# Kernel optimization log

Measured on AMD Instinct MI355X. Metric: run time of the kernel, lower is better.

Reference implementation:

```python
import jax, jax.numpy as jnp
import numpy as np

N_ENTITIES = 500_000
N_RELS = 1_000
EMB_DIM = 128
N_TRIPLES = 1_000_000

def setup_inputs() -> dict:
    key = jax.random.key(0)
    k1, k2, k3, k4, k5 = jax.random.split(key, 5)
    memory = jax.random.normal(k1, (N_ENTITIES, EMB_DIM), dtype=jnp.float32) * 0.1
    rel_table = jax.random.normal(k2, (N_RELS, EMB_DIM), dtype=jnp.float32)
    h_idx = jax.random.randint(k3, (N_TRIPLES,), 0, N_ENTITIES, dtype=jnp.int32)
    r_idx = jax.random.randint(k4, (N_TRIPLES,), 0, N_RELS, dtype=jnp.int32)
    t_idx = jax.random.randint(k5, (N_TRIPLES,), 0, N_ENTITIES, dtype=jnp.int32)
    return {"memory": memory, "rel_table": rel_table,
            "h_idx": h_idx, "r_idx": r_idx, "t_idx": t_idx}

def reference(memory, rel_table, h_idx, r_idx, t_idx):
    # Gather (all reads use the OLD memory, matching torch: RHS is computed
    # before the index_put).
    h_vec = memory[h_idx]          # [E, D]
    r_vec = rel_table[r_idx]       # [E, D]
    t_vec = memory[t_idx]          # [E, D]
    msg = h_vec + r_vec - t_vec
    new_vals = 0.9 * h_vec + 0.1 * msg   # = h_vec + 0.1*(r_vec - t_vec)
    # matching torch index_put(accumulate=False) semantics.
    return memory.at[h_idx].set(new_vals)
```

## Files before the change

### kernel.cpp

```cpp
#include <hip/hip_runtime.h>

#define N_ENTITIES 500000
#define N_RELS 1000
#define EMB_DIM 128
#define N_TRIPLES 1000000

typedef float floatx4 __attribute__((ext_vector_type(4)));


__global__ void init_winner_kernel(int* __restrict__ winner) {
    int i = blockIdx.x * blockDim.x + threadIdx.x;
    if (i < N_ENTITIES) winner[i] = -1;
}

__global__ void find_winner_kernel(const int* __restrict__ h_idx,
                                   int* __restrict__ winner) {
    int e = blockIdx.x * blockDim.x + threadIdx.x;
    if (e < N_TRIPLES) {
        atomicMax(&winner[h_idx[e]], e);
    }
}

__global__ void apply_kernel(const float* __restrict__ memory,
                             const float* __restrict__ rel_table,
                             const int* __restrict__ r_idx,
                             const int* __restrict__ t_idx,
                             const int* __restrict__ winner,
                             float* __restrict__ out) {
    int tid  = blockIdx.x * blockDim.x + threadIdx.x;
    int row  = tid >> 5;
    int lane = tid & 31;
    if (row >= N_ENTITIES) return;

    int w = winner[row];

    const floatx4* mrow = (const floatx4*)(memory + (size_t)row * EMB_DIM);
    floatx4 h = mrow[lane];

    floatx4 val = h;
    if (w >= 0) {
        int r = r_idx[w];
        int t = t_idx[w];
        floatx4 rv = ((const floatx4*)(rel_table + (size_t)r * EMB_DIM))[lane];
        floatx4 tv = ((const floatx4*)(memory   + (size_t)t * EMB_DIM))[lane];
        val = 0.9f * h + 0.1f * (h + rv - tv);
    }
    floatx4* orow = (floatx4*)(out + (size_t)row * EMB_DIM) + lane;
    __builtin_nontemporal_store(val, orow);
}

extern "C" void kernel_launch(void* const* d_in, const int* in_sizes, int n_in,
                              void* d_out, int out_size, void* d_ws, size_t ws_size,
                              hipStream_t stream) {
    const float* memory    = (const float*)d_in[0];
    const float* rel_table = (const float*)d_in[1];
    const int*   h_idx     = (const int*)d_in[2];
    const int*   r_idx     = (const int*)d_in[3];
    const int*   t_idx     = (const int*)d_in[4];
    float*       out       = (float*)d_out;

    int* winner = (int*)d_ws;

    {
        int threads = 256;
        int blocks = (N_ENTITIES + threads - 1) / threads;
        init_winner_kernel<<<blocks, threads, 0, stream>>>(winner);
    }
    {
        int threads = 256;
        int blocks = (N_TRIPLES + threads - 1) / threads;
        find_winner_kernel<<<blocks, threads, 0, stream>>>(h_idx, winner);
    }
    {
        int threads = 256;
        long long total = (long long)N_ENTITIES * 32;
        int blocks = (int)((total + threads - 1) / threads);
        apply_kernel<<<blocks, threads, 0, stream>>>(memory, rel_table, r_idx,
                                                     t_idx, winner, out);
    }
}
```

Measured before the change: 488.3 us.

## Pack winner triple index with r/t into 64-bit atomicMax key, batch rows per thread

The winner buffer now holds a 64-bit key per entity: the triple index (offset by one) in the high bits, with r and t packed below it. A single atomicMax therefore picks the last writer and records its r and t, so the apply kernel no longer makes the dependent r_idx/t_idx loads. The find kernel reads indices as int4 and handles four triples per thread. The apply kernel handles four rows per thread and issues their gathers together for more memory-level parallelism. It also always loads the rel and t rows, including row 0 for entities with no triple, and uses 64-bit atomics in place of 32-bit ones.

```diff
diff --git a/kernel.cpp b/kernel.cpp
--- a/kernel.cpp
+++ b/kernel.cpp
@@ -5,48 +5,72 @@
 #define EMB_DIM 128
 #define N_TRIPLES 1000000
 
+#define ROWS_PER_THREAD 4
+#define ROW_STRIDE (N_ENTITIES / ROWS_PER_THREAD)
+
 typedef float floatx4 __attribute__((ext_vector_type(4)));
+typedef unsigned long long u64;
 
 
-__global__ void init_winner_kernel(int* __restrict__ winner) {
+__global__ void init_pack_kernel(u64* __restrict__ pack) {
     int i = blockIdx.x * blockDim.x + threadIdx.x;
-    if (i < N_ENTITIES) winner[i] = -1;
+    if (i < N_ENTITIES) pack[i] = 0ull;
 }
 
-__global__ void find_winner_kernel(const int* __restrict__ h_idx,
-                                   int* __restrict__ winner) {
-    int e = blockIdx.x * blockDim.x + threadIdx.x;
-    if (e < N_TRIPLES) {
-        atomicMax(&winner[h_idx[e]], e);
-    }
+__global__ void find_winner_kernel(const int4* __restrict__ h4,
+                                   const int4* __restrict__ r4,
+                                   const int4* __restrict__ t4,
+                                   u64* __restrict__ pack) {
+    int q = blockIdx.x * blockDim.x + threadIdx.x;
+    if (q >= N_TRIPLES / 4) return;
+    int4 h = h4[q];
+    int4 r = r4[q];
+    int4 t = t4[q];
+    u64 e1 = (u64)(4 * q + 1);
+    atomicMax(&pack[h.x], (e1      << 29) | ((u64)r.x << 19) | (u64)t.x);
+    atomicMax(&pack[h.y], ((e1 + 1) << 29) | ((u64)r.y << 19) | (u64)t.y);
+    atomicMax(&pack[h.z], ((e1 + 2) << 29) | ((u64)r.z << 19) | (u64)t.z);
+    atomicMax(&pack[h.w], ((e1 + 3) << 29) | ((u64)r.w << 19) | (u64)t.w);
 }
 
 __global__ void apply_kernel(const float* __restrict__ memory,
                              const float* __restrict__ rel_table,
-                             const int* __restrict__ r_idx,
-                             const int* __restrict__ t_idx,
-                             const int* __restrict__ winner,
+                             const u64* __restrict__ pack,
                              float* __restrict__ out) {
     int tid  = blockIdx.x * blockDim.x + threadIdx.x;
-    int row  = tid >> 5;
+    int row0 = tid >> 5;
     int lane = tid & 31;
-    if (row >= N_ENTITIES) return;
+    if (row0 >= ROW_STRIDE) return;
 
-    int w = winner[row];
+    int rows[ROWS_PER_THREAD];
+    u64 k[ROWS_PER_THREAD];
+#pragma unroll
+    for (int i = 0; i < ROWS_PER_THREAD; ++i) {
+        rows[i] = row0 + i * ROW_STRIDE;
+        k[i] = pack[rows[i]];
+    }
 
-    const floatx4* mrow = (const floatx4*)(memory + (size_t)row * EMB_DIM);
-    floatx4 h = mrow[lane];
+    floatx4 h[ROWS_PER_THREAD];
+#pragma unroll
+    for (int i = 0; i < ROWS_PER_THREAD; ++i)
+        h[i] = ((const floatx4*)(memory + (size_t)rows[i] * EMB_DIM))[lane];
 
-    floatx4 val = h;
-    if (w >= 0) {
-        int r = r_idx[w];
-        int t = t_idx[w];
-        floatx4 rv = ((const floatx4*)(rel_table + (size_t)r * EMB_DIM))[lane];
-        floatx4 tv = ((const floatx4*)(memory   + (size_t)t * EMB_DIM))[lane];
-        val = 0.9f * h + 0.1f * (h + rv - tv);
+    floatx4 rv[ROWS_PER_THREAD], tv[ROWS_PER_THREAD];
+#pragma unroll
+    for (int i = 0; i < ROWS_PER_THREAD; ++i) {
+        int t = (int)(k[i] & 0x7FFFF);
+        int r = (int)((k[i] >> 19) & 0x3FF);
+        rv[i] = ((const floatx4*)(rel_table + (size_t)r * EMB_DIM))[lane];
+        tv[i] = ((const floatx4*)(memory    + (size_t)t * EMB_DIM))[lane];
     }
-    floatx4* orow = (floatx4*)(out + (size_t)row * EMB_DIM) + lane;
-    __builtin_nontemporal_store(val, orow);
+
+#pragma unroll
+    for (int i = 0; i < ROWS_PER_THREAD; ++i) {
+        floatx4 upd = 0.9f * h[i] + 0.1f * (h[i] + rv[i] - tv[i]);
+        floatx4 val = (k[i] != 0ull) ? upd : h[i];
+        floatx4* orow = (floatx4*)(out + (size_t)rows[i] * EMB_DIM) + lane;
+        __builtin_nontemporal_store(val, orow);
+    }
 }
 
 extern "C" void kernel_launch(void* const* d_in, const int* in_sizes, int n_in,
@@ -59,23 +83,24 @@
     const int*   t_idx     = (const int*)d_in[4];
     float*       out       = (float*)d_out;
 
-    int* winner = (int*)d_ws;
+    u64* pack = (u64*)d_ws;
 
     {
         int threads = 256;
         int blocks = (N_ENTITIES + threads - 1) / threads;
-        init_winner_kernel<<<blocks, threads, 0, stream>>>(winner);
+        init_pack_kernel<<<blocks, threads, 0, stream>>>(pack);
     }
     {
         int threads = 256;
-        int blocks = (N_TRIPLES + threads - 1) / threads;
-        find_winner_kernel<<<blocks, threads, 0, stream>>>(h_idx, winner);
+        int quads = N_TRIPLES / 4;
+        int blocks = (quads + threads - 1) / threads;
+        find_winner_kernel<<<blocks, threads, 0, stream>>>(
+            (const int4*)h_idx, (const int4*)r_idx, (const int4*)t_idx, pack);
     }
     {
         int threads = 256;
-        long long total = (long long)N_ENTITIES * 32;
+        long long total = (long long)ROW_STRIDE * 32;
         int blocks = (int)((total + threads - 1) / threads);
-        apply_kernel<<<blocks, threads, 0, stream>>>(memory, rel_table, r_idx,
-                                                     t_idx, winner, out);
+        apply_kernel<<<blocks, threads, 0, stream>>>(memory, rel_table, pack, out);
     }
 }
```

Result: no change. 488.8 us (+0.1%).
